# Performance work log

Hardware: AMD Instinct MI355X
Metric: run time of the kernel (lower is better)

## Reference

```python
import jax, jax.numpy as jnp
import numpy as np

K = 512          # num_embeddings
D = 8            # latent_dim
DECAY = 0.99     # ema_decay
EPS = 1e-5


def setup_inputs() -> dict:
    key = jax.random.key(0)
    k1, k2 = jax.random.split(key)
    z = jax.random.normal(k1, (64, D, 64, 64), dtype=jnp.float32)
    # codebook initialized uniform(-1/K, 1/K) as in the torch module
    codebook = jax.random.uniform(k2, (K, D), dtype=jnp.float32,
                                  minval=-1.0 / K, maxval=1.0 / K)
    ema_cluster_size = jnp.zeros((K,), dtype=jnp.float32)
    ema_w = jnp.zeros((K, D), dtype=jnp.float32)
    return {"z": z, "codebook": codebook,
            "ema_cluster_size": ema_cluster_size, "ema_w": ema_w}


def reference(z, codebook, ema_cluster_size, ema_w):
    B, C, H, W = z.shape
    # (B, HW, C) flattened latents, matching z.view(B,C,-1).permute(0,2,1)
    flat = z.reshape(B, C, H * W).transpose(0, 2, 1)

    # cdist p=2: ||z||^2 - 2 z.e + ||e||^2, then sqrt (argmin unaffected,
    # but we keep the sqrt for faithfulness to torch.cdist)
    z_sq = jnp.sum(flat * flat, axis=-1, keepdims=True)        # (B, N, 1)
    e_sq = jnp.sum(codebook * codebook, axis=-1)               # (K,)
    dots = jnp.einsum('bnd,kd->bnk', flat, codebook)           # (B, N, K)
    distances = jnp.sqrt(jnp.maximum(z_sq - 2.0 * dots + e_sq, 0.0))

    indices = jnp.argmin(distances, axis=-1)                   # (B, N) int

    # embedding gather with the OLD codebook (as in the torch forward)
    z_q = codebook[indices]                                    # (B, N, D)
    z_q = z_q.transpose(0, 2, 1).reshape(B, C, H, W)

    commitment_loss = jnp.mean((jax.lax.stop_gradient(z_q) - z) ** 2)
    loss = commitment_loss  # use_ema=True branch

    # ---- EMA in-place codebook update (buffers) ----
    idx_flat = indices.reshape(-1)                             # (B*N,)
    inp_flat = flat.reshape(-1, C)                             # (B*N, D)
    counts = jax.ops.segment_sum(jnp.ones_like(idx_flat, dtype=z.dtype),
                                 idx_flat, num_segments=K)     # (K,)
    sums = jax.ops.segment_sum(inp_flat, idx_flat, num_segments=K)  # (K, D)

    new_cs = ema_cluster_size * DECAY + counts * (1.0 - DECAY)
    new_w = ema_w * DECAY + sums * (1.0 - DECAY)
    n = jnp.sum(new_cs)
    cs_smoothed = (new_cs + EPS) / (n + K * EPS) * n
    new_codebook = new_w / cs_smoothed[:, None]

    return z_q, loss, new_codebook, cs_smoothed, new_w
```

## Files before the change

### kernel.cpp

```cpp
#include <hip/hip_runtime.h>

constexpr int Kc   = 512;
constexpr int Dc   = 8;
constexpr int HWc  = 4096;
constexpr int CHWc = Dc * HWc;
constexpr int Mc   = 64 * HWc;
constexpr int TOTALc = Mc * Dc;

constexpr int REP      = 8;
constexpr int RSTRIDE  = 4616;
constexpr int ACC_FLOATS = REP * RSTRIDE;

__global__ __launch_bounds__(256) void vq_prep(const float* __restrict__ cb,
                                               float* __restrict__ ws) {
    const int tid = blockIdx.x * 256 + threadIdx.x;
    float4* w4 = (float4*)ws;
    for (int i = tid; i < ACC_FLOATS / 4; i += gridDim.x * 256)
        w4[i] = float4{0.f, 0.f, 0.f, 0.f};
    if (blockIdx.x == 0) {
        for (int k = threadIdx.x; k < Kc; k += 256) {
            float s = 0.f;
#pragma unroll
            for (int c = 0; c < Dc; ++c) {
                const float e = cb[k * Dc + c];
                s = fmaf(e, e, s);
            }
            ws[ACC_FLOATS + k] = s;
        }
    }
}

__global__ __launch_bounds__(512, 8) void vq_main(const float* __restrict__ z,
                                                  const float* __restrict__ cb,
                                                  const float* __restrict__ esq,
                                                  float* __restrict__ ws,
                                                  float* __restrict__ zq) {
    __shared__ float s_counts[Kc];
    __shared__ float s_sums[Kc * Dc];
    __shared__ float s_mn[4][256];
    __shared__ int   s_im[4][256];
    __shared__ float s_loss;

    const int t = threadIdx.x;
    for (int i = t; i < Kc; i += 512) s_counts[i] = 0.f;
    for (int i = t; i < Kc * Dc; i += 512) s_sums[i] = 0.f;
    if (t == 0) s_loss = 0.f;

    const int vl = t & 127;
    const int g  = __builtin_amdgcn_readfirstlane(t >> 7);
    const int k0 = g << 7;

    const int base = blockIdx.x * 256;
    const int n0 = (base + vl) & (HWc - 1);
    const int b  = base >> 12;
    const float* zb = z + b * CHWc + n0;

    float zz0[Dc], zz1[Dc];
#pragma unroll
    for (int c = 0; c < Dc; ++c) {
        zz0[c] = -2.0f * zb[c * HWc];
        zz1[c] = -2.0f * zb[c * HWc + 128];
    }

    float mn0 = 3.4e38f, mn1 = 3.4e38f;
    int   i0 = k0, i1 = k0;
#pragma unroll 4
    for (int kk = 0; kk < 128; ++kk) {
        const int k = k0 + kk;
        float a0 = esq[k];
        float a1 = a0;
#pragma unroll
        for (int c = 0; c < Dc; ++c) {
            const float e = cb[k * Dc + c];
            a0 = fmaf(zz0[c], e, a0);
            a1 = fmaf(zz1[c], e, a1);
        }
        const bool c0 = a0 < mn0;
        mn0 = c0 ? a0 : mn0;
        i0  = c0 ? k  : i0;
        const bool c1 = a1 < mn1;
        mn1 = c1 ? a1 : mn1;
        i1  = c1 ? k  : i1;
    }
    s_mn[g][vl]       = mn0;
    s_im[g][vl]       = i0;
    s_mn[g][vl + 128] = mn1;
    s_im[g][vl + 128] = i1;
    __syncthreads();

    if (t < 256) {
        const int v = t;
        float mn = s_mn[0][v];
        int   im = s_im[0][v];
#pragma unroll
        for (int gg = 1; gg < 4; ++gg) {
            const float m2 = s_mn[gg][v];
            const int   j2 = s_im[gg][v];
            const bool  c2 = m2 < mn;
            mn = c2 ? m2 : mn;
            im = c2 ? j2 : im;
        }

        const float4* cb4 = (const float4*)cb;
        const float4 qa = cb4[im * 2], qb = cb4[im * 2 + 1];
        const float q[Dc] = {qa.x, qa.y, qa.z, qa.w, qb.x, qb.y, qb.z, qb.w};

        const int nv = (base + v) & (HWc - 1);
        const float* zv = z + b * CHWc + nv;
        float* zqv = zq + b * CHWc + nv;
        float lsum = 0.f;
        float zr[Dc];
#pragma unroll
        for (int c = 0; c < Dc; ++c) {
            zr[c] = zv[c * HWc];
            zqv[c * HWc] = q[c];
            const float d = q[c] - zr[c];
            lsum = fmaf(d, d, lsum);
        }

        unsafeAtomicAdd(&s_counts[im], 1.0f);
#pragma unroll
        for (int c = 0; c < Dc; ++c)
            unsafeAtomicAdd(&s_sums[im * Dc + c], zr[c]);
        unsafeAtomicAdd(&s_loss, lsum);
    }
    __syncthreads();

    float* acc = ws + (blockIdx.x & (REP - 1)) * RSTRIDE;
    for (int i = t; i < Kc; i += 512) {
        const float val = s_counts[i];
        if (val != 0.f) unsafeAtomicAdd(&acc[i], val);
    }
    for (int i = t; i < Kc * Dc; i += 512) {
        const float val = s_sums[i];
        if (val != 0.f) unsafeAtomicAdd(&acc[512 + i], val);
    }
    if (t == 0) unsafeAtomicAdd(&acc[4608], s_loss);
}

__global__ __launch_bounds__(512) void vq_final(const float* __restrict__ ws,
                                                const float* __restrict__ ema_cs,
                                                const float* __restrict__ ema_w,
                                                float* __restrict__ out) {
    constexpr float DEC  = 0.99f;
    constexpr float OMD  = (float)(1.0 - 0.99);
    constexpr float EPSf = 1e-5f;
    constexpr float KEPS = (float)(512 * 1e-5);
    __shared__ float red[512];
    __shared__ float s_cs[512];

    const int t = threadIdx.x;
    float cnt = 0.f;
#pragma unroll
    for (int r = 0; r < REP; ++r) cnt += ws[r * RSTRIDE + t];
    const float ncs = ema_cs[t] * DEC + cnt * OMD;
    red[t] = ncs;
    __syncthreads();
    for (int s = 256; s > 0; s >>= 1) {
        if (t < s) red[t] += red[t + s];
        __syncthreads();
    }
    const float n  = red[0];
    const float cs = (ncs + EPSf) / (n + KEPS) * n;
    s_cs[t] = cs;

    float* out_loss = out + TOTALc;
    float* out_cb   = out + TOTALc + 1;
    float* out_cs   = out_cb + Kc * Dc;
    float* out_nw   = out_cs + Kc;

    out_cs[t] = cs;
    __syncthreads();

    for (int e = t; e < Kc * Dc; e += 512) {
        float sm = 0.f;
#pragma unroll
        for (int r = 0; r < REP; ++r) sm += ws[r * RSTRIDE + 512 + e];
        const float nw = ema_w[e] * DEC + sm * OMD;
        out_nw[e] = nw;
        out_cb[e] = nw / s_cs[e >> 3];
    }
    if (t == 0) {
        float ls = 0.f;
#pragma unroll
        for (int r = 0; r < REP; ++r) ls += ws[r * RSTRIDE + 4608];
        out_loss[0] = ls * (1.0f / 2097152.0f);
    }
}

extern "C" void kernel_launch(void* const* d_in, const int* in_sizes, int n_in,
                              void* d_out, int out_size, void* d_ws, size_t ws_size,
                              hipStream_t stream) {
    const float* z      = (const float*)d_in[0];
    const float* cb     = (const float*)d_in[1];
    const float* ema_cs = (const float*)d_in[2];
    const float* ema_w  = (const float*)d_in[3];
    float* out = (float*)d_out;
    float* ws  = (float*)d_ws;

    vq_prep<<<32, 256, 0, stream>>>(cb, ws);
    vq_main<<<Mc / 256, 512, 0, stream>>>(z, cb, ws + ACC_FLOATS, ws, out);
    vq_final<<<1, 512, 0, stream>>>(ws, ema_cs, ema_w, out);
}
```

Baseline: 113.1 us.

## Give each thread one vector over full codebook and use direct global atomics

Each thread now computes the argmin for a single latent vector over all 512 codes, replacing the split across 4 thread groups and the shared-memory merge. The per-block shared histograms are removed; counts and sums are accumulated with global atomics per vector, and the loss uses a wavefront shuffle reduction. This removes barriers and LDS traffic but greatly increases global atomic contention and halves codebook-load reuse per thread.

```diff
diff --git a/kernel.cpp b/kernel.cpp
--- a/kernel.cpp
+++ b/kernel.cpp
@@ -30,112 +30,61 @@
     }
 }
 
-__global__ __launch_bounds__(512, 8) void vq_main(const float* __restrict__ z,
-                                                  const float* __restrict__ cb,
-                                                  const float* __restrict__ esq,
-                                                  float* __restrict__ ws,
-                                                  float* __restrict__ zq) {
-    __shared__ float s_counts[Kc];
-    __shared__ float s_sums[Kc * Dc];
-    __shared__ float s_mn[4][256];
-    __shared__ int   s_im[4][256];
-    __shared__ float s_loss;
-
-    const int t = threadIdx.x;
-    for (int i = t; i < Kc; i += 512) s_counts[i] = 0.f;
-    for (int i = t; i < Kc * Dc; i += 512) s_sums[i] = 0.f;
-    if (t == 0) s_loss = 0.f;
-
-    const int vl = t & 127;
-    const int g  = __builtin_amdgcn_readfirstlane(t >> 7);
-    const int k0 = g << 7;
-
-    const int base = blockIdx.x * 256;
-    const int n0 = (base + vl) & (HWc - 1);
-    const int b  = base >> 12;
+__global__ __launch_bounds__(256) void vq_main(const float* __restrict__ z,
+                                               const float* __restrict__ cb,
+                                               const float* __restrict__ esq,
+                                               float* __restrict__ ws,
+                                               float* __restrict__ zq) {
+    const int t   = threadIdx.x;
+    const int vid = blockIdx.x * 256 + t;
+    const int n0  = vid & (HWc - 1);
+    const int b   = vid >> 12;
     const float* zb = z + b * CHWc + n0;
 
-    float zz0[Dc], zz1[Dc];
+    float zr[Dc], zz[Dc];
 #pragma unroll
     for (int c = 0; c < Dc; ++c) {
-        zz0[c] = -2.0f * zb[c * HWc];
-        zz1[c] = -2.0f * zb[c * HWc + 128];
+        zr[c] = zb[c * HWc];
+        zz[c] = -2.0f * zr[c];
     }
 
-    float mn0 = 3.4e38f, mn1 = 3.4e38f;
-    int   i0 = k0, i1 = k0;
+    float mn = 3.4e38f;
+    int   im = 0;
 #pragma unroll 4
-    for (int kk = 0; kk < 128; ++kk) {
-        const int k = k0 + kk;
-        float a0 = esq[k];
-        float a1 = a0;
-#pragma unroll
-        for (int c = 0; c < Dc; ++c) {
-            const float e = cb[k * Dc + c];
-            a0 = fmaf(zz0[c], e, a0);
-            a1 = fmaf(zz1[c], e, a1);
-        }
-        const bool c0 = a0 < mn0;
-        mn0 = c0 ? a0 : mn0;
-        i0  = c0 ? k  : i0;
-        const bool c1 = a1 < mn1;
-        mn1 = c1 ? a1 : mn1;
-        i1  = c1 ? k  : i1;
-    }
-    s_mn[g][vl]       = mn0;
-    s_im[g][vl]       = i0;
-    s_mn[g][vl + 128] = mn1;
-    s_im[g][vl + 128] = i1;
-    __syncthreads();
-
-    if (t < 256) {
-        const int v = t;
-        float mn = s_mn[0][v];
-        int   im = s_im[0][v];
-#pragma unroll
-        for (int gg = 1; gg < 4; ++gg) {
-            const float m2 = s_mn[gg][v];
-            const int   j2 = s_im[gg][v];
-            const bool  c2 = m2 < mn;
-            mn = c2 ? m2 : mn;
-            im = c2 ? j2 : im;
-        }
-
-        const float4* cb4 = (const float4*)cb;
-        const float4 qa = cb4[im * 2], qb = cb4[im * 2 + 1];
-        const float q[Dc] = {qa.x, qa.y, qa.z, qa.w, qb.x, qb.y, qb.z, qb.w};
-
-        const int nv = (base + v) & (HWc - 1);
-        const float* zv = z + b * CHWc + nv;
-        float* zqv = zq + b * CHWc + nv;
-        float lsum = 0.f;
-        float zr[Dc];
-#pragma unroll
-        for (int c = 0; c < Dc; ++c) {
-            zr[c] = zv[c * HWc];
-            zqv[c * HWc] = q[c];
-            const float d = q[c] - zr[c];
-            lsum = fmaf(d, d, lsum);
-        }
-
-        unsafeAtomicAdd(&s_counts[im], 1.0f);
+    for (int k = 0; k < Kc; ++k) {
+        float a = esq[k];
 #pragma unroll
         for (int c = 0; c < Dc; ++c)
-            unsafeAtomicAdd(&s_sums[im * Dc + c], zr[c]);
-        unsafeAtomicAdd(&s_loss, lsum);
+            a = fmaf(zz[c], cb[k * Dc + c], a);
+        const bool cl = a < mn;
+        mn = cl ? a : mn;
+        im = cl ? k : im;
     }
-    __syncthreads();
+
+    const float4* cb4 = (const float4*)cb;
+    const float4 qa = cb4[im * 2], qb = cb4[im * 2 + 1];
+    const float q[Dc] = {qa.x, qa.y, qa.z, qa.w, qb.x, qb.y, qb.z, qb.w};
+
+    float* zqv = zq + b * CHWc + n0;
+    float lsum = 0.f;
+#pragma unroll
+    for (int c = 0; c < Dc; ++c) {
+        zqv[c * HWc] = q[c];
+        const float d = q[c] - zr[c];
+        lsum = fmaf(d, d, lsum);
+    }
 
     float* acc = ws + (blockIdx.x & (REP - 1)) * RSTRIDE;
-    for (int i = t; i < Kc; i += 512) {
-        const float val = s_counts[i];
-        if (val != 0.f) unsafeAtomicAdd(&acc[i], val);
-    }
-    for (int i = t; i < Kc * Dc; i += 512) {
-        const float val = s_sums[i];
-        if (val != 0.f) unsafeAtomicAdd(&acc[512 + i], val);
-    }
-    if (t == 0) unsafeAtomicAdd(&acc[4608], s_loss);
+    unsafeAtomicAdd(&acc[im], 1.0f);
+#pragma unroll
+    for (int c = 0; c < Dc; ++c)
+        unsafeAtomicAdd(&acc[512 + im * Dc + c], zr[c]);
+
+#pragma unroll
+    for (int s = 32; s > 0; s >>= 1)
+        lsum += __shfl_down(lsum, s);
+    if ((t & 63) == 0)
+        unsafeAtomicAdd(&acc[4608], lsum);
 }
 
 __global__ __launch_bounds__(512) void vq_final(const float* __restrict__ ws,
@@ -199,6 +148,6 @@
     float* ws  = (float*)d_ws;
 
     vq_prep<<<32, 256, 0, stream>>>(cb, ws);
-    vq_main<<<Mc / 256, 512, 0, stream>>>(z, cb, ws + ACC_FLOATS, ws, out);
+    vq_main<<<Mc / 256, 256, 0, stream>>>(z, cb, ws + ACC_FLOATS, ws, out);
     vq_final<<<1, 512, 0, stream>>>(ws, ema_cs, ema_w, out);
 }
```

Result: slower. 333.1 us (+194.5%).

## Register-block four points per thread over eight codebook groups, compute esq in-block

Applied to the files above, without the earlier changes.

Each thread now scores four latent vectors against a 64-entry codebook slice, with eight wave groups covering the 512 entries, instead of two vectors against 128 entries. Each codebook row load is reused across four points, cutting scalar or L1 codebook traffic per FMA. The codebook squared norms are now computed per block into shared memory instead of in the prep kernel. The trade-off is more registers per thread under the 512x8 launch bound, and the cross-group argmin reduction grows from four to eight steps.

```diff
diff --git a/kernel.cpp b/kernel.cpp
--- a/kernel.cpp
+++ b/kernel.cpp
@@ -11,34 +11,22 @@
 constexpr int RSTRIDE  = 4616;
 constexpr int ACC_FLOATS = REP * RSTRIDE;
 
-__global__ __launch_bounds__(256) void vq_prep(const float* __restrict__ cb,
-                                               float* __restrict__ ws) {
+__global__ __launch_bounds__(256) void vq_prep(float* __restrict__ ws) {
     const int tid = blockIdx.x * 256 + threadIdx.x;
     float4* w4 = (float4*)ws;
     for (int i = tid; i < ACC_FLOATS / 4; i += gridDim.x * 256)
         w4[i] = float4{0.f, 0.f, 0.f, 0.f};
-    if (blockIdx.x == 0) {
-        for (int k = threadIdx.x; k < Kc; k += 256) {
-            float s = 0.f;
-#pragma unroll
-            for (int c = 0; c < Dc; ++c) {
-                const float e = cb[k * Dc + c];
-                s = fmaf(e, e, s);
-            }
-            ws[ACC_FLOATS + k] = s;
-        }
-    }
 }
 
 __global__ __launch_bounds__(512, 8) void vq_main(const float* __restrict__ z,
                                                   const float* __restrict__ cb,
-                                                  const float* __restrict__ esq,
                                                   float* __restrict__ ws,
                                                   float* __restrict__ zq) {
+    __shared__ float s_esq[Kc];
+    __shared__ float s_mn[8][256];
+    __shared__ int   s_im[8][256];
     __shared__ float s_counts[Kc];
     __shared__ float s_sums[Kc * Dc];
-    __shared__ float s_mn[4][256];
-    __shared__ int   s_im[4][256];
     __shared__ float s_loss;
 
     const int t = threadIdx.x;
@@ -46,66 +34,82 @@
     for (int i = t; i < Kc * Dc; i += 512) s_sums[i] = 0.f;
     if (t == 0) s_loss = 0.f;
 
-    const int vl = t & 127;
-    const int g  = __builtin_amdgcn_readfirstlane(t >> 7);
-    const int k0 = g << 7;
+    {
+        const float4* cb4 = (const float4*)cb;
+        const float4 ea = cb4[t * 2], eb = cb4[t * 2 + 1];
+        float s = 0.f;
+        s = fmaf(ea.x, ea.x, s); s = fmaf(ea.y, ea.y, s);
+        s = fmaf(ea.z, ea.z, s); s = fmaf(ea.w, ea.w, s);
+        s = fmaf(eb.x, eb.x, s); s = fmaf(eb.y, eb.y, s);
+        s = fmaf(eb.z, eb.z, s); s = fmaf(eb.w, eb.w, s);
+        s_esq[t] = s;
+    }
+
+    const int l = t & 63;
+    const int g  = __builtin_amdgcn_readfirstlane(t >> 6);
+    const int k0 = g << 6;
 
     const int base = blockIdx.x * 256;
-    const int n0 = (base + vl) & (HWc - 1);
     const int b  = base >> 12;
+    const int n0 = (base & (HWc - 1)) + l;
     const float* zb = z + b * CHWc + n0;
 
-    float zz0[Dc], zz1[Dc];
-#pragma unroll
-    for (int c = 0; c < Dc; ++c) {
-        zz0[c] = -2.0f * zb[c * HWc];
-        zz1[c] = -2.0f * zb[c * HWc + 128];
-    }
-
-    float mn0 = 3.4e38f, mn1 = 3.4e38f;
-    int   i0 = k0, i1 = k0;
-#pragma unroll 4
-    for (int kk = 0; kk < 128; ++kk) {
+    float zz[4][Dc];
+#pragma unroll
+    for (int j = 0; j < 4; ++j)
+#pragma unroll
+        for (int c = 0; c < Dc; ++c)
+            zz[j][c] = -2.0f * zb[c * HWc + 64 * j];
+
+    __syncthreads();
+
+    float mn[4] = {3.4e38f, 3.4e38f, 3.4e38f, 3.4e38f};
+    int   im[4] = {k0, k0, k0, k0};
+#pragma unroll 2
+    for (int kk = 0; kk < 64; ++kk) {
         const int k = k0 + kk;
-        float a0 = esq[k];
-        float a1 = a0;
-#pragma unroll
-        for (int c = 0; c < Dc; ++c) {
-            const float e = cb[k * Dc + c];
-            a0 = fmaf(zz0[c], e, a0);
-            a1 = fmaf(zz1[c], e, a1);
+        const float ev = s_esq[k];
+        float e[Dc];
+#pragma unroll
+        for (int c = 0; c < Dc; ++c) e[c] = cb[k * Dc + c];
+        float a[4] = {ev, ev, ev, ev};
+#pragma unroll
+        for (int c = 0; c < Dc; ++c)
+#pragma unroll
+            for (int j = 0; j < 4; ++j)
+                a[j] = fmaf(zz[j][c], e[c], a[j]);
+#pragma unroll
+        for (int j = 0; j < 4; ++j) {
+            const bool cl = a[j] < mn[j];
+            mn[j] = cl ? a[j] : mn[j];
+            im[j] = cl ? k    : im[j];
         }
-        const bool c0 = a0 < mn0;
-        mn0 = c0 ? a0 : mn0;
-        i0  = c0 ? k  : i0;
-        const bool c1 = a1 < mn1;
-        mn1 = c1 ? a1 : mn1;
-        i1  = c1 ? k  : i1;
-    }
-    s_mn[g][vl]       = mn0;
-    s_im[g][vl]       = i0;
-    s_mn[g][vl + 128] = mn1;
-    s_im[g][vl + 128] = i1;
+    }
+#pragma unroll
+    for (int j = 0; j < 4; ++j) {
+        s_mn[g][l + 64 * j] = mn[j];
+        s_im[g][l + 64 * j] = im[j];
+    }
     __syncthreads();
 
     if (t < 256) {
         const int v = t;
-        float mn = s_mn[0][v];
-        int   im = s_im[0][v];
-#pragma unroll
-        for (int gg = 1; gg < 4; ++gg) {
+        float mnv = s_mn[0][v];
+        int   imv = s_im[0][v];
+#pragma unroll
+        for (int gg = 1; gg < 8; ++gg) {
             const float m2 = s_mn[gg][v];
             const int   j2 = s_im[gg][v];
-            const bool  c2 = m2 < mn;
-            mn = c2 ? m2 : mn;
-            im = c2 ? j2 : im;
+            const bool  c2 = m2 < mnv;
+            mnv = c2 ? m2 : mnv;
+            imv = c2 ? j2 : imv;
         }
 
         const float4* cb4 = (const float4*)cb;
-        const float4 qa = cb4[im * 2], qb = cb4[im * 2 + 1];
+        const float4 qa = cb4[imv * 2], qb = cb4[imv * 2 + 1];
         const float q[Dc] = {qa.x, qa.y, qa.z, qa.w, qb.x, qb.y, qb.z, qb.w};
 
-        const int nv = (base + v) & (HWc - 1);
+        const int nv = (base & (HWc - 1)) + v;
         const float* zv = z + b * CHWc + nv;
         float* zqv = zq + b * CHWc + nv;
         float lsum = 0.f;
@@ -118,10 +122,10 @@
             lsum = fmaf(d, d, lsum);
         }
 
-        unsafeAtomicAdd(&s_counts[im], 1.0f);
+        unsafeAtomicAdd(&s_counts[imv], 1.0f);
 #pragma unroll
         for (int c = 0; c < Dc; ++c)
-            unsafeAtomicAdd(&s_sums[im * Dc + c], zr[c]);
+            unsafeAtomicAdd(&s_sums[imv * Dc + c], zr[c]);
         unsafeAtomicAdd(&s_loss, lsum);
     }
     __syncthreads();
@@ -198,7 +202,7 @@
     float* out = (float*)d_out;
     float* ws  = (float*)d_ws;
 
-    vq_prep<<<32, 256, 0, stream>>>(cb, ws);
-    vq_main<<<Mc / 256, 512, 0, stream>>>(z, cb, ws + ACC_FLOATS, ws, out);
+    vq_prep<<<32, 256, 0, stream>>>(ws);
+    vq_main<<<Mc / 256, 512, 0, stream>>>(z, cb, ws, out);
     vq_final<<<1, 512, 0, stream>>>(ws, ema_cs, ema_w, out);
 }
```

Measured after the change: 117.8 us. +4.1%, slower.

## Use packed FMA over 4 points per thread with 8 codebook groups; parallelize final

Applied to the files above, without the earlier changes.

The distance search now assigns each thread 4 latent vectors across 8 wave-uniform codebook slices of 64 entries. Each thread uses inline-asm v_pk_fma_f32 with codebook pairs read as 64-bit scalar operands, so each packed FMA updates two points at once. The cross-group argmin merge grows from 4 to 8 partials. The finalize kernel is spread over 9 blocks instead of 1, and each block recomputes the cluster-size reduction. The aim is to raise FMA throughput in the dominant distance loop, at the cost of relying on hand-written asm correctness and doing redundant reduction work in the finalize blocks.

```diff
diff --git a/kernel.cpp b/kernel.cpp
--- a/kernel.cpp
+++ b/kernel.cpp
@@ -10,6 +10,8 @@
 constexpr int REP      = 8;
 constexpr int RSTRIDE  = 4616;
 constexpr int ACC_FLOATS = REP * RSTRIDE;
+
+typedef float v2f __attribute__((ext_vector_type(2)));
 
 __global__ __launch_bounds__(256) void vq_prep(const float* __restrict__ cb,
                                                float* __restrict__ ws) {
@@ -35,10 +37,10 @@
                                                   const float* __restrict__ esq,
                                                   float* __restrict__ ws,
                                                   float* __restrict__ zq) {
+    __shared__ float s_mn[8][256];
+    __shared__ int   s_im[8][256];
     __shared__ float s_counts[Kc];
     __shared__ float s_sums[Kc * Dc];
-    __shared__ float s_mn[4][256];
-    __shared__ int   s_im[4][256];
     __shared__ float s_loss;
 
     const int t = threadIdx.x;
@@ -46,46 +48,59 @@
     for (int i = t; i < Kc * Dc; i += 512) s_sums[i] = 0.f;
     if (t == 0) s_loss = 0.f;
 
-    const int vl = t & 127;
-    const int g  = __builtin_amdgcn_readfirstlane(t >> 7);
-    const int k0 = g << 7;
+    const int l = t & 63;
+    const int g  = __builtin_amdgcn_readfirstlane(t >> 6);
+    const int k0 = g << 6;
 
     const int base = blockIdx.x * 256;
-    const int n0 = (base + vl) & (HWc - 1);
     const int b  = base >> 12;
+    const int n0 = (base & (HWc - 1)) + l;
     const float* zb = z + b * CHWc + n0;
 
-    float zz0[Dc], zz1[Dc];
+    v2f zzA[Dc], zzB[Dc];
 #pragma unroll
     for (int c = 0; c < Dc; ++c) {
-        zz0[c] = -2.0f * zb[c * HWc];
-        zz1[c] = -2.0f * zb[c * HWc + 128];
-    }
-
-    float mn0 = 3.4e38f, mn1 = 3.4e38f;
-    int   i0 = k0, i1 = k0;
-#pragma unroll 4
-    for (int kk = 0; kk < 128; ++kk) {
+        zzA[c] = v2f{-2.0f * zb[c * HWc],       -2.0f * zb[c * HWc + 64]};
+        zzB[c] = v2f{-2.0f * zb[c * HWc + 128], -2.0f * zb[c * HWc + 192]};
+    }
+
+    const unsigned long long* cbq = (const unsigned long long*)cb;
+
+    float mn0 = 3.4e38f, mn1 = 3.4e38f, mn2 = 3.4e38f, mn3 = 3.4e38f;
+    int   i0 = k0, i1 = k0, i2 = k0, i3 = k0;
+#pragma unroll 2
+    for (int kk = 0; kk < 64; ++kk) {
         const int k = k0 + kk;
-        float a0 = esq[k];
-        float a1 = a0;
-#pragma unroll
-        for (int c = 0; c < Dc; ++c) {
-            const float e = cb[k * Dc + c];
-            a0 = fmaf(zz0[c], e, a0);
-            a1 = fmaf(zz1[c], e, a1);
-        }
-        const bool c0 = a0 < mn0;
-        mn0 = c0 ? a0 : mn0;
-        i0  = c0 ? k  : i0;
-        const bool c1 = a1 < mn1;
-        mn1 = c1 ? a1 : mn1;
-        i1  = c1 ? k  : i1;
-    }
-    s_mn[g][vl]       = mn0;
-    s_im[g][vl]       = i0;
-    s_mn[g][vl + 128] = mn1;
-    s_im[g][vl + 128] = i1;
+        const unsigned long long q0 = cbq[4 * k + 0];
+        const unsigned long long q1 = cbq[4 * k + 1];
+        const unsigned long long q2 = cbq[4 * k + 2];
+        const unsigned long long q3 = cbq[4 * k + 3];
+        const float ev = esq[k];
+        v2f aA = {ev, ev};
+        v2f aB = {ev, ev};
+#define PKSTEP(Q, P0, P1)                                              \
+        asm("v_pk_fma_f32 %0, %2, %4, %0 op_sel_hi:[1,0,1]\n\t"        \
+            "v_pk_fma_f32 %1, %3, %4, %1 op_sel_hi:[1,0,1]\n\t"        \
+            "v_pk_fma_f32 %0, %5, %4, %0 op_sel:[0,1,0]\n\t"           \
+            "v_pk_fma_f32 %1, %6, %4, %1 op_sel:[0,1,0]"               \
+            : "+v"(aA), "+v"(aB)                                       \
+            : "v"(zzA[P0]), "v"(zzB[P0]), "s"(Q), "v"(zzA[P1]), "v"(zzB[P1]))
+        PKSTEP(q0, 0, 1);
+        PKSTEP(q1, 2, 3);
+        PKSTEP(q2, 4, 5);
+        PKSTEP(q3, 6, 7);
+#undef PKSTEP
+        const float a0 = aA.x, a1 = aA.y, a2 = aB.x, a3 = aB.y;
+        bool c;
+        c = a0 < mn0; mn0 = c ? a0 : mn0; i0 = c ? k : i0;
+        c = a1 < mn1; mn1 = c ? a1 : mn1; i1 = c ? k : i1;
+        c = a2 < mn2; mn2 = c ? a2 : mn2; i2 = c ? k : i2;
+        c = a3 < mn3; mn3 = c ? a3 : mn3; i3 = c ? k : i3;
+    }
+    s_mn[g][l]       = mn0;  s_im[g][l]       = i0;
+    s_mn[g][l +  64] = mn1;  s_im[g][l +  64] = i1;
+    s_mn[g][l + 128] = mn2;  s_im[g][l + 128] = i2;
+    s_mn[g][l + 192] = mn3;  s_im[g][l + 192] = i3;
     __syncthreads();
 
     if (t < 256) {
@@ -93,7 +108,7 @@
         float mn = s_mn[0][v];
         int   im = s_im[0][v];
 #pragma unroll
-        for (int gg = 1; gg < 4; ++gg) {
+        for (int gg = 1; gg < 8; ++gg) {
             const float m2 = s_mn[gg][v];
             const int   j2 = s_im[gg][v];
             const bool  c2 = m2 < mn;
@@ -105,7 +120,7 @@
         const float4 qa = cb4[im * 2], qb = cb4[im * 2 + 1];
         const float q[Dc] = {qa.x, qa.y, qa.z, qa.w, qb.x, qb.y, qb.z, qb.w};
 
-        const int nv = (base + v) & (HWc - 1);
+        const int nv = (base & (HWc - 1)) + v;
         const float* zv = z + b * CHWc + nv;
         float* zqv = zq + b * CHWc + nv;
         float lsum = 0.f;
@@ -169,22 +184,25 @@
     float* out_cs   = out_cb + Kc * Dc;
     float* out_nw   = out_cs + Kc;
 
-    out_cs[t] = cs;
-    __syncthreads();
-
-    for (int e = t; e < Kc * Dc; e += 512) {
+    __syncthreads();
+
+    const int blk = blockIdx.x;
+    if (blk == 0) {
+        out_cs[t] = cs;
+        if (t == 0) {
+            float ls = 0.f;
+#pragma unroll
+            for (int r = 0; r < REP; ++r) ls += ws[r * RSTRIDE + 4608];
+            out_loss[0] = ls * (1.0f / 2097152.0f);
+        }
+    } else {
+        const int e = (blk - 1) * 512 + t;
         float sm = 0.f;
 #pragma unroll
         for (int r = 0; r < REP; ++r) sm += ws[r * RSTRIDE + 512 + e];
         const float nw = ema_w[e] * DEC + sm * OMD;
         out_nw[e] = nw;
         out_cb[e] = nw / s_cs[e >> 3];
-    }
-    if (t == 0) {
-        float ls = 0.f;
-#pragma unroll
-        for (int r = 0; r < REP; ++r) ls += ws[r * RSTRIDE + 4608];
-        out_loss[0] = ls * (1.0f / 2097152.0f);
     }
 }
 
@@ -200,5 +218,5 @@
 
     vq_prep<<<32, 256, 0, stream>>>(cb, ws);
     vq_main<<<Mc / 256, 512, 0, stream>>>(z, cb, ws + ACC_FLOATS, ws, out);
-    vq_final<<<1, 512, 0, stream>>>(ws, ema_cs, ema_w, out);
-}
+    vq_final<<<9, 512, 0, stream>>>(ws, ema_cs, ema_w, out);
+}
```

Result: faster. 109.6 us (-3.1%).
